# Optimization experiments

Measured on AMD Instinct MI355X. Metric: run time of the kernel, lower is better.

## Reference

```python
import jax, jax.numpy as jnp
import numpy as np

B, T, D = 2, 2048, 1024
H = 16
DH = D // H            # 64, per-head dim
C = 128                # d_kv_compress
ROPE_BASE = 10000.0


def _rope_cos_sin(t_len, d_head, dtype):
    # freqs: (T, d_head/2); emb = cat(freqs, freqs) -> (T, d_head)
    inv_freq = 1.0 / (ROPE_BASE ** (jnp.arange(0, d_head, 2, dtype=jnp.float32) / d_head))
    freqs = jnp.arange(t_len, dtype=jnp.float32)[:, None] * inv_freq[None, :]
    emb = jnp.concatenate([freqs, freqs], axis=-1)
    return jnp.cos(emb).astype(dtype), jnp.sin(emb).astype(dtype)


def _rotate_half(x):
    x1, x2 = jnp.split(x, 2, axis=-1)
    return jnp.concatenate([-x2, x1], axis=-1)


def _apply_rope(x, cos, sin):
    # x: (B,H,T,DH); cos/sin: (T,DH)
    return x * cos[None, None] + _rotate_half(x) * sin[None, None]


def setup_inputs() -> dict:
    key = jax.random.key(0)
    ks = jax.random.split(key, 12)
    s = 0.02
    return {
        "x": jax.random.normal(ks[0], (B, T, D), dtype=jnp.float32),
        "w_dk": jax.random.normal(ks[1], (D, C), dtype=jnp.float32) * s,
        "b_dk": jnp.zeros((C,), dtype=jnp.float32),
        "w_dv": jax.random.normal(ks[2], (D, C), dtype=jnp.float32) * s,
        "b_dv": jnp.zeros((C,), dtype=jnp.float32),
        "w_uk": jax.random.normal(ks[3], (C, D), dtype=jnp.float32) * s,
        "b_uk": jnp.zeros((D,), dtype=jnp.float32),
        "w_uv": jax.random.normal(ks[4], (C, D), dtype=jnp.float32) * s,
        "b_uv": jnp.zeros((D,), dtype=jnp.float32),
        "w_o": jax.random.normal(ks[5], (D, D), dtype=jnp.float32) * s,
        "b_o": jnp.zeros((D,), dtype=jnp.float32),
    }


def reference(x, w_dk, b_dk, w_dv, b_dv, w_uk, b_uk, w_uv, b_uv, w_o, b_o):
    Bx, Tx, Dx = x.shape
    # low-rank KV compression then up-projection
    c_k = x @ w_dk + b_dk                      # (B,T,C)
    c_v = x @ w_dv + b_dv                      # (B,T,C)
    k = c_k @ w_uk + b_uk                      # (B,T,D)
    v = c_v @ w_uv + b_uv                      # (B,T,D)

    def split_heads(t):  # (B,T,D) -> (B,H,T,DH)
        return t.reshape(Bx, Tx, H, DH).transpose(0, 2, 1, 3)

    q = split_heads(x)
    k = split_heads(k)
    v = split_heads(v)

    cos, sin = _rope_cos_sin(Tx, DH, x.dtype)
    q = _apply_rope(q, cos, sin)
    k = _apply_rope(k, cos, sin)

    scale = 1.0 / np.sqrt(DH)
    attn = jnp.einsum('bhid,bhjd->bhij', q, k) * scale
    attn = jax.nn.softmax(attn, axis=-1)
    out = jnp.einsum('bhij,bhjd->bhid', attn, v)   # (B,H,T,DH)
    out = out.transpose(0, 2, 1, 3).reshape(Bx, Tx, Dx)
    return out @ w_o + b_o
```

## Files before the change

### kernel.cpp

```cpp
#include <hip/hip_runtime.h>
#include <hip/hip_bf16.h>
#include <math.h>

constexpr int kB  = 2;
constexpr int kT  = 2048;
constexpr int kD  = 1024;
constexpr int kH  = 16;
constexpr int kDH = 64;
constexpr int kC  = 128;
constexpr int kM  = kB * kT;
constexpr int kBH = kB * kH;

#define LOG10000_OVER_32 0.28782313662425575f
#define QSCALE 0.1803368801111773f

typedef unsigned short ushort_t;
using short8 = __attribute__((ext_vector_type(8))) short;
using f32x4  = __attribute__((ext_vector_type(4))) float;

__device__ inline ushort_t f2bf(float f) {
    __hip_bfloat16 h = __float2bfloat16(f);
    return *reinterpret_cast<ushort_t*>(&h);
}

__device__ inline short8 cvt8(const float* p) {
    float4 f0 = *reinterpret_cast<const float4*>(p);
    float4 f1 = *reinterpret_cast<const float4*>(p + 4);
    short8 v;
    v[0] = (short)f2bf(f0.x); v[1] = (short)f2bf(f0.y);
    v[2] = (short)f2bf(f0.z); v[3] = (short)f2bf(f0.w);
    v[4] = (short)f2bf(f1.x); v[5] = (short)f2bf(f1.y);
    v[6] = (short)f2bf(f1.z); v[7] = (short)f2bf(f1.w);
    return v;
}

__global__ __launch_bounds__(256)
void wtrans(const float* __restrict__ w_dk, const float* __restrict__ w_dv,
            const float* __restrict__ w_uk, const float* __restrict__ w_uv,
            const float* __restrict__ w_o,
            ushort_t* __restrict__ dkT, ushort_t* __restrict__ dvT,
            ushort_t* __restrict__ ukT, ushort_t* __restrict__ uvT,
            ushort_t* __restrict__ oT, float2* __restrict__ tab) {
    if (blockIdx.z == 5) {
        int flat = blockIdx.y * 32 + blockIdx.x;
        if (flat >= kT / 8) return;
        int t = flat * 8 + (threadIdx.x >> 5);
        int i = threadIdx.x & 31;
        float inv_freq = expf(-(float)i * LOG10000_OVER_32);
        float s, c;
        sincosf((float)t * inv_freq, &s, &c);
        tab[t * 32 + i] = make_float2(c, s);
        return;
    }
    const float* src; ushort_t* dst; int R, C;
    switch (blockIdx.z) {
        case 0: src = w_dk; dst = dkT; R = kD; C = kC; break;
        case 1: src = w_dv; dst = dvT; R = kD; C = kC; break;
        case 2: src = w_uk; dst = ukT; R = kC; C = kD; break;
        case 3: src = w_uv; dst = uvT; R = kC; C = kD; break;
        default: src = w_o; dst = oT;  R = kD; C = kD; break;
    }
    int c0 = blockIdx.x * 32, r0 = blockIdx.y * 32;
    if (c0 >= C || r0 >= R) return;

    __shared__ float Tl[32][33];
    int tx = threadIdx.x & 31, ty = threadIdx.x >> 5;
#pragma unroll
    for (int i = 0; i < 4; ++i)
        Tl[ty + 8 * i][tx] = src[(size_t)(r0 + ty + 8 * i) * C + c0 + tx];
    __syncthreads();
#pragma unroll
    for (int i = 0; i < 4; ++i)
        dst[(size_t)(c0 + ty + 8 * i) * R + r0 + tx] = f2bf(Tl[tx][ty + 8 * i]);
}

template<int MODE0, int MODE1>
__global__ __launch_bounds__(256)
void gemm_mfma(const ushort_t* __restrict__ A0_, const ushort_t* __restrict__ A1_,
               const ushort_t* __restrict__ Wt0, const float* __restrict__ bias0, void* __restrict__ C0,
               const ushort_t* __restrict__ Wt1, const float* __restrict__ bias1, void* __restrict__ C1,
               const float2* __restrict__ tab, int M, int N, int K) {
    constexpr int LDT = 40;
    __shared__ __align__(16) ushort_t As[128 * LDT];
    __shared__ __align__(16) ushort_t Bs[128 * LDT];

    const ushort_t* A    = blockIdx.z ? A1_ : A0_;
    const ushort_t* Wt   = blockIdx.z ? Wt1 : Wt0;
    const float*    bias = blockIdx.z ? bias1 : bias0;
    void*           Cc   = blockIdx.z ? C1 : C0;
    const int       mode = blockIdx.z ? MODE1 : MODE0;

    const int tid  = threadIdx.x;
    const int wave = tid >> 6, lane = tid & 63;
    const int g = lane >> 4, cl = lane & 15;
    const int m0 = blockIdx.y * 128, n0 = blockIdx.x * 128;
    const int wm = (wave >> 1) * 64, wn = (wave & 1) * 64;

    const int ar = tid >> 1;
    const int ac = (tid & 1) * 16;

    f32x4 acc[4][4] = {};

    for (int k0 = 0; k0 < K; k0 += 32) {
        {
            const ushort_t* Ab = A + (size_t)(m0 + ar) * K + k0 + ac;
            *reinterpret_cast<short8*>(&As[ar * LDT + ac])     = *reinterpret_cast<const short8*>(Ab);
            *reinterpret_cast<short8*>(&As[ar * LDT + ac + 8]) = *reinterpret_cast<const short8*>(Ab + 8);
            const ushort_t* Wb = Wt + (size_t)(n0 + ar) * K + k0 + ac;
            *reinterpret_cast<short8*>(&Bs[ar * LDT + ac])     = *reinterpret_cast<const short8*>(Wb);
            *reinterpret_cast<short8*>(&Bs[ar * LDT + ac + 8]) = *reinterpret_cast<const short8*>(Wb + 8);
        }
        __syncthreads();

        short8 a[4], b[4];
#pragma unroll
        for (int mi = 0; mi < 4; ++mi)
            a[mi] = *reinterpret_cast<const short8*>(&As[(wm + mi * 16 + cl) * LDT + g * 8]);
#pragma unroll
        for (int ni = 0; ni < 4; ++ni)
            b[ni] = *reinterpret_cast<const short8*>(&Bs[(wn + ni * 16 + cl) * LDT + g * 8]);
#pragma unroll
        for (int mi = 0; mi < 4; ++mi)
#pragma unroll
            for (int ni = 0; ni < 4; ++ni)
                acc[mi][ni] = __builtin_amdgcn_mfma_f32_16x16x32_bf16(a[mi], b[ni], acc[mi][ni], 0, 0, 0);
        __syncthreads();
    }

#pragma unroll
    for (int mi = 0; mi < 4; ++mi) {
        if (mode == 4) {
            const int h = (n0 + wn) >> 6;
#pragma unroll
            for (int r = 0; r < 4; ++r) {
                const int m = m0 + wm + mi * 16 + 4 * g + r;
                const int bb = m >> 11, t = m & (kT - 1);
                ushort_t* kp = (ushort_t*)Cc + (((size_t)bb * kH + h) * kT + t) * kDH;
#pragma unroll
                for (int pr = 0; pr < 2; ++pr) {
                    const int i = pr * 16 + cl;
                    float2 cs = tab[t * 32 + i];
                    float v1 = acc[mi][pr][r]     + bias[n0 + wn + pr * 16 + cl];
                    float v2 = acc[mi][pr + 2][r] + bias[n0 + wn + (pr + 2) * 16 + cl];
                    kp[i]      = f2bf(v1 * cs.x - v2 * cs.y);
                    kp[i + 32] = f2bf(v2 * cs.x + v1 * cs.y);
                }
            }
        } else {
#pragma unroll
            for (int ni = 0; ni < 4; ++ni) {
                const int mb = m0 + wm + mi * 16 + 4 * g;
                const int nn = n0 + wn + ni * 16 + cl;
                const float bv = bias[nn];
                const int h = nn >> 6, d = nn & (kDH - 1);
                const int bb = mb >> 11, t0 = mb & (kT - 1);
                uint2 u;
                u.x = (unsigned int)f2bf(acc[mi][ni][0] + bv) | ((unsigned int)f2bf(acc[mi][ni][1] + bv) << 16);
                u.y = (unsigned int)f2bf(acc[mi][ni][2] + bv) | ((unsigned int)f2bf(acc[mi][ni][3] + bv) << 16);
                ushort_t* vt = (ushort_t*)Cc;
                *reinterpret_cast<uint2*>(&vt[(((size_t)bb * kH + h) * kDH + d) * kT + t0]) = u;
            }
        }
    }
}

template<bool AF32, int MODE>
__global__ __launch_bounds__(256)
void gemm64(const void* __restrict__ A0_, const void* __restrict__ A1_,
            const ushort_t* __restrict__ Wt0, const float* __restrict__ bias0, void* __restrict__ C0,
            const ushort_t* __restrict__ Wt1, const float* __restrict__ bias1, void* __restrict__ C1,
            int M, int N, int K) {
    constexpr int LDT = 40;
    __shared__ __align__(16) ushort_t As[128 * LDT];
    __shared__ __align__(16) ushort_t Bs[64 * LDT];

    const void*     A    = blockIdx.z ? A1_ : A0_;
    const ushort_t* Wt   = blockIdx.z ? Wt1 : Wt0;
    const float*    bias = blockIdx.z ? bias1 : bias0;
    void*           Cc   = blockIdx.z ? C1 : C0;

    const int tid  = threadIdx.x;
    const int wave = tid >> 6, lane = tid & 63;
    const int g = lane >> 4, cl = lane & 15;
    const int m0 = blockIdx.y * 128, n0 = blockIdx.x * 64;
    const int wm = (wave >> 1) * 64, wn = (wave & 1) * 32;

    const int ar = tid >> 1, ac = (tid & 1) * 16;
    const int br = tid >> 2, bc = (tid & 3) * 8;

    f32x4 acc[4][2] = {};

    for (int k0 = 0; k0 < K; k0 += 32) {
        if constexpr (AF32) {
            const float* Af = (const float*)A + (size_t)(m0 + ar) * K + k0 + ac;
            *reinterpret_cast<short8*>(&As[ar * LDT + ac])     = cvt8(Af);
            *reinterpret_cast<short8*>(&As[ar * LDT + ac + 8]) = cvt8(Af + 8);
        } else {
            const ushort_t* Ab = (const ushort_t*)A + (size_t)(m0 + ar) * K + k0 + ac;
            *reinterpret_cast<short8*>(&As[ar * LDT + ac])     = *reinterpret_cast<const short8*>(Ab);
            *reinterpret_cast<short8*>(&As[ar * LDT + ac + 8]) = *reinterpret_cast<const short8*>(Ab + 8);
        }
        *reinterpret_cast<short8*>(&Bs[br * LDT + bc]) =
            *reinterpret_cast<const short8*>(Wt + (size_t)(n0 + br) * K + k0 + bc);
        __syncthreads();

        short8 a[4], b[2];
#pragma unroll
        for (int mi = 0; mi < 4; ++mi)
            a[mi] = *reinterpret_cast<const short8*>(&As[(wm + mi * 16 + cl) * LDT + g * 8]);
#pragma unroll
        for (int ni = 0; ni < 2; ++ni)
            b[ni] = *reinterpret_cast<const short8*>(&Bs[(wn + ni * 16 + cl) * LDT + g * 8]);
#pragma unroll
        for (int mi = 0; mi < 4; ++mi)
#pragma unroll
            for (int ni = 0; ni < 2; ++ni)
                acc[mi][ni] = __builtin_amdgcn_mfma_f32_16x16x32_bf16(a[mi], b[ni], acc[mi][ni], 0, 0, 0);
        __syncthreads();
    }

#pragma unroll
    for (int mi = 0; mi < 4; ++mi)
#pragma unroll
        for (int ni = 0; ni < 2; ++ni) {
            const int mb = m0 + wm + mi * 16 + 4 * g;
            const int nn = n0 + wn + ni * 16 + cl;
            const float bv = bias[nn];
            if constexpr (MODE == 0) {
#pragma unroll
                for (int r = 0; r < 4; ++r)
                    ((float*)Cc)[(size_t)(mb + r) * N + nn] = acc[mi][ni][r] + bv;
            } else {
#pragma unroll
                for (int r = 0; r < 4; ++r)
                    ((ushort_t*)Cc)[(size_t)(mb + r) * N + nn] = f2bf(acc[mi][ni][r] + bv);
            }
        }
}

__global__ __launch_bounds__(256)
void attn_mfma(const float* __restrict__ x, const float2* __restrict__ tab,
               const ushort_t* __restrict__ k_bf, const ushort_t* __restrict__ vt_bf,
               ushort_t* __restrict__ att_bf) {
    constexpr int LDK = 72;
    constexpr int LDV = 40;
    constexpr int LDP = 36;
    const int blk  = blockIdx.x;
    const int bh   = (blk & 7) * 4 + ((blk >> 3) & 3);
    const int qt   = blk >> 5;
    const int tid  = threadIdx.x;
    const int wave = tid >> 6, lane = tid & 63;
    const int g = lane >> 4, c = lane & 15;
    const int qbase = qt * 64 + wave * 16;
    const int b = bh >> 4, h = bh & (kH - 1);

    __shared__ __align__(16) ushort_t Ks[2][32 * LDK];
    __shared__ __align__(16) ushort_t Vs[2][64 * LDV];
    __shared__ __align__(16) ushort_t P_lds[4][16 * LDP];
    ushort_t* P = P_lds[wave];

    short8 qa0, qa1;
    {
        const int t = qbase + c;
        const float* xp = x + ((size_t)(b * kT + t)) * kD + h * kDH + g * 8;
        float xa[8], xb[8]; float2 cs[8];
        *reinterpret_cast<float4*>(&xa[0]) = *reinterpret_cast<const float4*>(xp);
        *reinterpret_cast<float4*>(&xa[4]) = *reinterpret_cast<const float4*>(xp + 4);
        *reinterpret_cast<float4*>(&xb[0]) = *reinterpret_cast<const float4*>(xp + 32);
        *reinterpret_cast<float4*>(&xb[4]) = *reinterpret_cast<const float4*>(xp + 36);
        const float2* tp = tab + (size_t)t * 32 + g * 8;
#pragma unroll
        for (int j = 0; j < 8; j += 2)
            *reinterpret_cast<float4*>(&cs[j]) = *reinterpret_cast<const float4*>(tp + j);
#pragma unroll
        for (int j = 0; j < 8; ++j) {
            qa0[j] = (short)f2bf((xa[j] * cs[j].x - xb[j] * cs[j].y) * QSCALE);
            qa1[j] = (short)f2bf((xb[j] * cs[j].x + xa[j] * cs[j].y) * QSCALE);
        }
    }

    const ushort_t* kb = k_bf + (size_t)bh * kT * kDH;
    const ushort_t* vb = vt_bf + (size_t)bh * kDH * kT;

    const int kr_ = tid >> 3, kc_ = (tid & 7) * 8;
    const int vr_ = tid >> 2, vc_ = (tid & 3) * 8;

    {
        short8 kreg = *reinterpret_cast<const short8*>(&kb[(size_t)kr_ * kDH + kc_]);
        short8 vreg = *reinterpret_cast<const short8*>(&vb[(size_t)vr_ * kT + vc_]);
        *reinterpret_cast<short8*>(&Ks[0][kr_ * LDK + kc_]) = kreg;
        *reinterpret_cast<short8*>(&Vs[0][vr_ * LDV + vc_]) = vreg;
    }
    __syncthreads();

    f32x4 acc[4] = {};
    float lsum[4] = {};

    for (int kt = 0; kt < kT; kt += 32) {
        const int cur = (kt >> 5) & 1;
        short8 kreg, vreg;
        const bool more = (kt + 32) < kT;
        if (more) {
            kreg = *reinterpret_cast<const short8*>(&kb[(size_t)(kt + 32 + kr_) * kDH + kc_]);
            vreg = *reinterpret_cast<const short8*>(&vb[(size_t)vr_ * kT + kt + 32 + vc_]);
        }

        short8 kf[2][2];
#pragma unroll
        for (int kj = 0; kj < 2; ++kj)
#pragma unroll
            for (int f = 0; f < 2; ++f)
                kf[kj][f] = *reinterpret_cast<const short8*>(&Ks[cur][(kj * 16 + c) * LDK + f * 32 + g * 8]);

        f32x4 z = {0.f, 0.f, 0.f, 0.f};
        f32x4 s0 = __builtin_amdgcn_mfma_f32_16x16x32_bf16(qa0, kf[0][0], z, 0, 0, 0);
        s0 = __builtin_amdgcn_mfma_f32_16x16x32_bf16(qa1, kf[0][1], s0, 0, 0, 0);
        f32x4 s1 = __builtin_amdgcn_mfma_f32_16x16x32_bf16(qa0, kf[1][0], z, 0, 0, 0);
        s1 = __builtin_amdgcn_mfma_f32_16x16x32_bf16(qa1, kf[1][1], s1, 0, 0, 0);

#pragma unroll
        for (int r = 0; r < 4; ++r) {
            float p0 = exp2f(s0[r]);
            float p1 = exp2f(s1[r]);
            lsum[r] += p0 + p1;
            P[(4 * g + r) * LDP + c]      = f2bf(p0);
            P[(4 * g + r) * LDP + 16 + c] = f2bf(p1);
        }
        short8 pa = *reinterpret_cast<const short8*>(&P[c * LDP + g * 8]);

        short8 vf[4];
#pragma unroll
        for (int n = 0; n < 4; ++n)
            vf[n] = *reinterpret_cast<const short8*>(&Vs[cur][(16 * n + c) * LDV + g * 8]);
#pragma unroll
        for (int n = 0; n < 4; ++n)
            acc[n] = __builtin_amdgcn_mfma_f32_16x16x32_bf16(pa, vf[n], acc[n], 0, 0, 0);

        if (more) {
            *reinterpret_cast<short8*>(&Ks[cur ^ 1][kr_ * LDK + kc_]) = kreg;
            *reinterpret_cast<short8*>(&Vs[cur ^ 1][vr_ * LDV + vc_]) = vreg;
        }
        __syncthreads();
    }

#pragma unroll
    for (int off = 1; off < 16; off <<= 1)
#pragma unroll
        for (int r = 0; r < 4; ++r)
            lsum[r] += __shfl_xor(lsum[r], off, 64);

#pragma unroll
    for (int r = 0; r < 4; ++r) {
        float inv_l = 1.0f / lsum[r];
        size_t row = (size_t)(b * kT + qbase + 4 * g + r) * kD + h * kDH;
#pragma unroll
        for (int n = 0; n < 4; ++n)
            att_bf[row + 16 * n + c] = f2bf(acc[n][r] * inv_l);
    }
}

extern "C" void kernel_launch(void* const* d_in, const int* in_sizes, int n_in,
                              void* d_out, int out_size, void* d_ws, size_t ws_size,
                              hipStream_t stream) {
    const float* x    = (const float*)d_in[0];
    const float* w_dk = (const float*)d_in[1];
    const float* b_dk = (const float*)d_in[2];
    const float* w_dv = (const float*)d_in[3];
    const float* b_dv = (const float*)d_in[4];
    const float* w_uk = (const float*)d_in[5];
    const float* b_uk = (const float*)d_in[6];
    const float* w_uv = (const float*)d_in[7];
    const float* b_uv = (const float*)d_in[8];
    const float* w_o  = (const float*)d_in[9];
    const float* b_o  = (const float*)d_in[10];
    float* out = (float*)d_out;

    char* w = (char*)d_ws;
    ushort_t* k_bf   = (ushort_t*)w;  w += (size_t)kM * kD * 2;
    ushort_t* vt_bf  = (ushort_t*)w;  w += (size_t)kM * kD * 2;
    ushort_t* att_bf = (ushort_t*)w;  w += (size_t)kM * kD * 2;
    ushort_t* ckbf   = (ushort_t*)w;  w += (size_t)kM * kC * 2;
    ushort_t* cvbf   = (ushort_t*)w;  w += (size_t)kM * kC * 2;
    ushort_t* dkT    = (ushort_t*)w;  w += (size_t)kC * kD * 2;
    ushort_t* dvT    = (ushort_t*)w;  w += (size_t)kC * kD * 2;
    ushort_t* ukT    = (ushort_t*)w;  w += (size_t)kD * kC * 2;
    ushort_t* uvT    = (ushort_t*)w;  w += (size_t)kD * kC * 2;
    ushort_t* oT     = (ushort_t*)w;  w += (size_t)kD * kD * 2;
    float2*   tab    = (float2*)w;    w += (size_t)kT * 32 * 8;

    dim3 blk(256);

    wtrans<<<dim3(32, 32, 6), blk, 0, stream>>>(w_dk, w_dv, w_uk, w_uv, w_o,
                                                dkT, dvT, ukT, uvT, oT, tab);

    gemm64<true, 3><<<dim3(kC / 64, kM / 128, 2), blk, 0, stream>>>(
        x, x, dkT, b_dk, ckbf, dvT, b_dv, cvbf, kM, kC, kD);

    gemm_mfma<4, 2><<<dim3(kD / 128, kM / 128, 2), blk, 0, stream>>>(
        ckbf, cvbf, ukT, b_uk, k_bf, uvT, b_uv, vt_bf, tab, kM, kD, kC);

    attn_mfma<<<dim3(kT / 64 * kBH), blk, 0, stream>>>(x, tab, k_bf, vt_bf, att_bf);

    gemm64<false, 0><<<dim3(kD / 64, kM / 128, 1), blk, 0, stream>>>(
        att_bf, att_bf, oT, b_o, out, oT, b_o, out, kM, kD, kD);
}
```

Baseline: 249.0 us.

## Load V fragments directly from global, single-buffer XOR-swizzled K tile

V^T fragments are now read straight from global memory into registers instead of being staged through shared memory. K is staged in one unpadded, XOR-swizzled LDS buffer rather than a padded double buffer, so the register prefetch of the next tile is gone. This cuts LDS footprint and staging traffic, but it exposes global-load latency each iteration, since nothing is prefetched and there is an extra barrier per tile.

After: 281.7 us. +13.1%, slower.

```diff
diff --git a/kernel.cpp b/kernel.cpp
--- a/kernel.cpp
+++ b/kernel.cpp
@@ -242,8 +242,6 @@
 void attn_mfma(const float* __restrict__ x, const float2* __restrict__ tab,
                const ushort_t* __restrict__ k_bf, const ushort_t* __restrict__ vt_bf,
                ushort_t* __restrict__ att_bf) {
-    constexpr int LDK = 72;
-    constexpr int LDV = 40;
     constexpr int LDP = 36;
     const int blk  = blockIdx.x;
     const int bh   = (blk & 7) * 4 + ((blk >> 3) & 3);
@@ -254,8 +252,7 @@
     const int qbase = qt * 64 + wave * 16;
     const int b = bh >> 4, h = bh & (kH - 1);
 
-    __shared__ __align__(16) ushort_t Ks[2][32 * LDK];
-    __shared__ __align__(16) ushort_t Vs[2][64 * LDV];
+    __shared__ __align__(16) ushort_t Ks[32 * 64];
     __shared__ __align__(16) ushort_t P_lds[4][16 * LDP];
     ushort_t* P = P_lds[wave];
 
@@ -283,34 +280,31 @@
     const ushort_t* vb = vt_bf + (size_t)bh * kDH * kT;
 
     const int kr_ = tid >> 3, kc_ = (tid & 7) * 8;
-    const int vr_ = tid >> 2, vc_ = (tid & 3) * 8;
-
-    {
-        short8 kreg = *reinterpret_cast<const short8*>(&kb[(size_t)kr_ * kDH + kc_]);
-        short8 vreg = *reinterpret_cast<const short8*>(&vb[(size_t)vr_ * kT + vc_]);
-        *reinterpret_cast<short8*>(&Ks[0][kr_ * LDK + kc_]) = kreg;
-        *reinterpret_cast<short8*>(&Vs[0][vr_ * LDV + vc_]) = vreg;
-    }
-    __syncthreads();
+    const int ksw = kr_ * 64 + (kc_ ^ ((kr_ & 7) << 3));
 
     f32x4 acc[4] = {};
     float lsum[4] = {};
 
     for (int kt = 0; kt < kT; kt += 32) {
-        const int cur = (kt >> 5) & 1;
-        short8 kreg, vreg;
-        const bool more = (kt + 32) < kT;
-        if (more) {
-            kreg = *reinterpret_cast<const short8*>(&kb[(size_t)(kt + 32 + kr_) * kDH + kc_]);
-            vreg = *reinterpret_cast<const short8*>(&vb[(size_t)vr_ * kT + kt + 32 + vc_]);
-        }
+        *reinterpret_cast<short8*>(&Ks[ksw]) =
+            *reinterpret_cast<const short8*>(&kb[(size_t)(kt + kr_) * kDH + kc_]);
+        __syncthreads();
+
+        short8 vf[4];
+#pragma unroll
+        for (int n = 0; n < 4; ++n)
+            vf[n] = *reinterpret_cast<const short8*>(&vb[(size_t)(16 * n + c) * kT + kt + g * 8]);
 
         short8 kf[2][2];
 #pragma unroll
         for (int kj = 0; kj < 2; ++kj)
 #pragma unroll
-            for (int f = 0; f < 2; ++f)
-                kf[kj][f] = *reinterpret_cast<const short8*>(&Ks[cur][(kj * 16 + c) * LDK + f * 32 + g * 8]);
+            for (int f = 0; f < 2; ++f) {
+                const int row = kj * 16 + c;
+                const int col = f * 32 + g * 8;
+                kf[kj][f] = *reinterpret_cast<const short8*>(
+                    &Ks[row * 64 + (col ^ ((row & 7) << 3))]);
+            }
 
         f32x4 z = {0.f, 0.f, 0.f, 0.f};
         f32x4 s0 = __builtin_amdgcn_mfma_f32_16x16x32_bf16(qa0, kf[0][0], z, 0, 0, 0);
@@ -328,18 +322,9 @@
         }
         short8 pa = *reinterpret_cast<const short8*>(&P[c * LDP + g * 8]);
 
-        short8 vf[4];
-#pragma unroll
-        for (int n = 0; n < 4; ++n)
-            vf[n] = *reinterpret_cast<const short8*>(&Vs[cur][(16 * n + c) * LDV + g * 8]);
 #pragma unroll
         for (int n = 0; n < 4; ++n)
             acc[n] = __builtin_amdgcn_mfma_f32_16x16x32_bf16(pa, vf[n], acc[n], 0, 0, 0);
-
-        if (more) {
-            *reinterpret_cast<short8*>(&Ks[cur ^ 1][kr_ * LDK + kc_]) = kreg;
-            *reinterpret_cast<short8*>(&Vs[cur ^ 1][vr_ * LDV + vc_]) = vreg;
-        }
         __syncthreads();
     }
 
```
